# Kernel tuning notes

Measured on AMD Instinct MI355X. Metric: run time of the kernel, lower is better.

## Reference

```python
import jax, jax.numpy as jnp
import numpy as np

B, C, H, W = 4, 128, 64, 64
THITA = 1e-4


def conv1x1(x, w, b):
    # 1x1 conv + bias + ReLU; x:[B,Cin,H,W], w:[Cout,Cin], b:[Cout]
    return jax.nn.relu(jnp.einsum('bihw,oi->bohw', x, w) + b[None, :, None, None])


_CONV_SPECS = [
    ('neighbor', 2 * C, 4),
    ('pro_key', C, C), ('pro_val', C, C),
    ('lat_key', C, C), ('lat_val', C, C),
    ('tmp1', C, 2 * C),
    ('now1', C, 2),
    ('now_key', C, C), ('now_val', C, C),
    ('q', C, C), ('k', C, C), ('v', C, C),
]


def setup_inputs() -> dict:
    key = jax.random.key(0)
    ks = jax.random.split(key, 1 + 2 * len(_CONV_SPECS))
    inp = {'event': jax.random.normal(ks[0], (B, 6, H, W), dtype=jnp.float32)}
    i = 1
    for name, o, c in _CONV_SPECS:
        s = 1.0 / np.sqrt(c)
        inp['w_' + name] = jax.random.uniform(ks[i], (o, c), minval=-s, maxval=s, dtype=jnp.float32)
        inp['b_' + name] = jax.random.uniform(ks[i + 1], (o,), minval=-s, maxval=s, dtype=jnp.float32)
        i += 2
    return inp


def reference(event, w_neighbor, b_neighbor, w_pro_key, b_pro_key, w_pro_val, b_pro_val,
              w_lat_key, b_lat_key, w_lat_val, b_lat_val, w_tmp1, b_tmp1,
              w_now1, b_now1, w_now_key, b_now_key, w_now_val, b_now_val,
              w_q, b_q, w_k, b_k, w_v, b_v):
    pro, now, lat = event[:, 0:2], event[:, 2:4], event[:, 4:6]
    neigh = conv1x1(jnp.concatenate([pro, lat], axis=1), w_neighbor, b_neighbor)  # [B,2C,H,W]
    pro_key = conv1x1(neigh[:, :C], w_pro_key, b_pro_key)
    pro_val = conv1x1(neigh[:, C:], w_pro_val, b_pro_val)
    lat_key = conv1x1(neigh[:, :C], w_lat_key, b_lat_key)
    lat_val = conv1x1(neigh[:, C:], w_lat_val, b_lat_val)
    # NOTE: source applies conv_tmp1 (shared weights) to both key and val paths
    key_n = conv1x1(jnp.concatenate([pro_key, lat_key], axis=1), w_tmp1, b_tmp1)
    val_n = conv1x1(jnp.concatenate([pro_val, lat_val], axis=1), w_tmp1, b_tmp1)
    now_f = conv1x1(now, w_now1, b_now1)
    now_key = conv1x1(now_f, w_now_key, b_now_key)
    now_val = conv1x1(now_f, w_now_val, b_now_val)
    N = H * W
    q = conv1x1(key_n, w_q, b_q).reshape(B, C, N)          # proj_query pre-permute
    k = conv1x1(now_key, w_k, b_k).reshape(B, C, N)        # [B,C,N]
    attn = jax.nn.softmax(jnp.einsum('bcn,bcm->bnm', q, k), axis=-1)  # [B,N,N]
    v = conv1x1(val_n, w_v, b_v).reshape(B, C, N)
    out = jnp.einsum('bcm,bnm->bcn', v, attn).reshape(B, C, H, W)
    return THITA * out + now_val
```

## Files before the change

kernel.cpp:

```cpp
#include <hip/hip_runtime.h>

#define B_ 4
#define C_ 128
#define N_ 4096
#define LOG2E 1.44269504088896340736f

typedef __attribute__((ext_vector_type(8))) __bf16 bf16x8;
typedef __attribute__((ext_vector_type(16))) float f32x16;

#define SWZ(n) (((n) & 15) << 4)

__device__ __forceinline__ unsigned short cvb(float x) {
    return __builtin_bit_cast(unsigned short, (__bf16)x);
}
__device__ __forceinline__ unsigned pk2(float lo, float hi) {
    return (unsigned)cvb(lo) | ((unsigned)cvb(hi) << 16);
}
__device__ __forceinline__ float bfu(unsigned short u) {
    return __builtin_bit_cast(float, (unsigned)u << 16);
}
__device__ __forceinline__ float fexp2(float x) {
#if __has_builtin(__builtin_amdgcn_exp2f)
    return __builtin_amdgcn_exp2f(x);
#else
    float r;
    asm("v_exp_f32 %0, %1" : "=v"(r) : "v"(x));
    return r;
#endif
}
__device__ inline void gload_lds16(const void* g, void* l) {
    __builtin_amdgcn_global_load_lds(
        (const __attribute__((address_space(1))) unsigned int*)g,
        (__attribute__((address_space(3))) unsigned int*)l, 16, 0, 0);
}
__device__ __forceinline__ void plswapf(float& a, float& b) {
    asm volatile("v_permlane32_swap_b32 %0, %1" : "+v"(a), "+v"(b));
}
__device__ __forceinline__ void plswapu(unsigned& a, unsigned& b) {
    asm volatile("v_permlane32_swap_b32 %0, %1" : "+v"(a), "+v"(b));
}

__global__ __launch_bounds__(256) void k_wcvt(
        const float* pk, const float* lk, const float* pv, const float* lv,
        const float* t1, const float* nk, const float* nv,
        const float* q, const float* k, const float* v,
        const float* bpk, const float* blk, const float* bpv, const float* blv,
        const float* bnk, const float* bnv,
        unsigned short* Wk, unsigned short* Wv, unsigned short* Wt1,
        unsigned short* Wnow, unsigned short* Wq, unsigned short* Wkk,
        unsigned short* Wvv, float* bck, float* bcv, float* bcn) {
    int i = blockIdx.x * 256 + threadIdx.x;
    if (i < 22528) {
        int c = i;
        const float *s0, *s1 = nullptr;
        unsigned short* dst;
        int ks;
        if      (c < 4096)  { dst = Wk;   ks = 3; s0 = pk; s1 = lk; }
        else if (c < 8192)  { dst = Wv;   ks = 3; s0 = pv; s1 = lv; c -= 4096; }
        else if (c < 12288) { dst = Wt1;  ks = 4; s0 = t1;          c -= 8192; }
        else if (c < 16384) { dst = Wnow; ks = 3; s0 = nk; s1 = nv; c -= 12288; }
        else if (c < 18432) { dst = Wq;   ks = 3; s0 = q;           c -= 16384; }
        else if (c < 20480) { dst = Wkk;  ks = 3; s0 = k;           c -= 18432; }
        else                { dst = Wvv;  ks = 3; s0 = v;           c -= 20480; }
        int K = 16 << ks;
        int lane = c & 63, tile = c >> 6;
        int mt = tile >> ks, kt = tile & ((1 << ks) - 1);
        int row = mt * 32 + (lane & 31);
        int col = kt * 16 + (lane >> 5) * 8;
        const float* src = (s1 && row >= 128) ? (s1 + (size_t)(row - 128) * K + col)
                                              : (s0 + (size_t)row * K + col);
        unsigned short ov[8];
        #pragma unroll
        for (int j = 0; j < 8; ++j) ov[j] = cvb(src[j]);
        *(uint4*)(dst + (size_t)c * 8) = *(const uint4*)ov;
    }
    else if (i < 22784) { int j = i - 22528; bck[j] = j < 128 ? bpk[j] : blk[j - 128]; }
    else if (i < 23040) { int j = i - 22784; bcv[j] = j < 128 ? bpv[j] : blv[j - 128]; }
    else if (i < 23296) { int j = i - 23040; bcn[j] = j < 128 ? bnk[j] : bnv[j - 128]; }
}

template<int KSTEPS, int ROWB>
__device__ __forceinline__ f32x16 gtile(const char* Ab, int aChBase,
        const unsigned short* Wf, int mchunk, int nl, int h) {
    f32x16 acc;
    #pragma unroll
    for (int r = 0; r < 16; ++r) acc[r] = 0.f;
    const char* arow = Ab + nl * ROWB;
    const unsigned short* wb = Wf + ((size_t)mchunk * KSTEPS) * 512 + (nl + 32 * h) * 8;
    #pragma unroll
    for (int kk = 0; kk < KSTEPS; ++kk) {
        bf16x8 a = *(const bf16x8*)(arow + ((aChBase + kk * 32 + h * 16) ^ SWZ(nl)));
        bf16x8 wf = *(const bf16x8*)(wb + kk * 512);
        acc = __builtin_amdgcn_mfma_f32_32x32x16_bf16(a, wf, acc, 0, 0, 0);
    }
    return acc;
}

__device__ __forceinline__ void epi_lds(char* dst, int rowB, f32x16 acc,
        const float* bias, int m0, int nl, int h) {
    int m = m0 + nl;
    float bs = bias[m];
    #pragma unroll
    for (int r = 0; r < 16; ++r) {
        int n = (r & 3) + 8 * (r >> 2) + 4 * h;
        *(unsigned short*)(dst + n * rowB + ((m * 2) ^ SWZ(n))) =
            cvb(fmaxf(acc[r] + bs, 0.f));
    }
}

__device__ __forceinline__ void epi_nc(unsigned short* Y, f32x16 acc,
        const float* bias, float scale, int m0, int n0g, int b, int nl, int h) {
    int m = m0 + nl;
    float bs = bias[m];
    #pragma unroll
    for (int r = 0; r < 16; ++r) {
        int n = (r & 3) + 8 * (r >> 2) + 4 * h;
        Y[((size_t)b * N_ + n0g + n) * C_ + m] = cvb(fmaxf(acc[r] + bs, 0.f) * scale);
    }
}

__device__ __forceinline__ void epi_cn_b16(unsigned short* Y, f32x16 acc,
        const float* bias, int m0, int n0g, int b, int nl, int h) {
    int m = m0 + nl;
    float bs = bias[m];
    #pragma unroll
    for (int r2 = 0; r2 < 4; ++r2) {
        int nn = 8 * r2 + 4 * h;
        uint2 o;
        o.x = pk2(fmaxf(acc[4*r2+0] + bs, 0.f), fmaxf(acc[4*r2+1] + bs, 0.f));
        o.y = pk2(fmaxf(acc[4*r2+2] + bs, 0.f), fmaxf(acc[4*r2+3] + bs, 0.f));
        *(uint2*)(Y + ((size_t)b * C_ + m) * N_ + n0g + nn) = o;
    }
}

__device__ __forceinline__ void epi_cn_f32(float* Y, f32x16 acc,
        const float* bias, int m0, int n0g, int b, int nl, int h) {
    int m = m0 + nl;
    float bs = bias[m];
    #pragma unroll
    for (int r2 = 0; r2 < 4; ++r2) {
        int nn = 8 * r2 + 4 * h;
        float4 o;
        o.x = fmaxf(acc[4*r2+0] + bs, 0.f);
        o.y = fmaxf(acc[4*r2+1] + bs, 0.f);
        o.z = fmaxf(acc[4*r2+2] + bs, 0.f);
        o.w = fmaxf(acc[4*r2+3] + bs, 0.f);
        *(float4*)(Y + ((size_t)b * C_ + m) * N_ + n0g + nn) = o;
    }
}

__global__ __launch_bounds__(256) void k_chain(
        const float* __restrict__ ev, const float* __restrict__ w_nb,
        const float* __restrict__ b_nb, const float* __restrict__ w_n1,
        const float* __restrict__ b_n1,
        const unsigned short* __restrict__ Wk, const unsigned short* __restrict__ Wv,
        const unsigned short* __restrict__ Wt1, const unsigned short* __restrict__ Wnow,
        const unsigned short* __restrict__ Wq, const unsigned short* __restrict__ Wkk,
        const unsigned short* __restrict__ Wvv,
        const float* __restrict__ bck, const float* __restrict__ bcv,
        const float* __restrict__ bt1, const float* __restrict__ bcn,
        const float* __restrict__ bq, const float* __restrict__ bk,
        const float* __restrict__ bv,
        unsigned short* __restrict__ Qt, unsigned short* __restrict__ Kb,
        unsigned short* __restrict__ Vb, float* __restrict__ NowV) {
    __shared__ char lds[57344];
    char* NEIGH = lds;
    char* KCAT  = lds + 16384;
    char* VCAT  = lds + 32768;
    char* NOWF  = lds + 49152;
    char* KEYN  = lds;
    char* VALN  = lds + 8192;
    char* NOWK  = lds + 16384;

    const int t = threadIdx.x, lane = t & 63, w = t >> 6;
    const int nl = lane & 31, h = lane >> 5;
    const int b = blockIdx.y;
    const int n0g = blockIdx.x * 32;
    const int m0 = w * 32;
    const int mc = w;

    {
        int n = t & 31, grp = t >> 5;
        const float* evb = ev + (size_t)b * 6 * N_ + n0g + n;
        float e0 = evb[0], e1 = evb[N_], e4 = evb[4*N_], e5 = evb[5*N_];
        float e2 = evb[2*N_], e3 = evb[3*N_];
        int och0 = grp * 32;
        #pragma unroll
        for (int i = 0; i < 32; i += 4) {
            float r_[4];
            #pragma unroll
            for (int j = 0; j < 4; ++j) {
                int o = och0 + i + j;
                float4 w4 = *(const float4*)(w_nb + o * 4);
                r_[j] = fmaxf(b_nb[o] + w4.x*e0 + w4.y*e1 + w4.z*e4 + w4.w*e5, 0.f);
            }
            uint2 val; val.x = pk2(r_[0], r_[1]); val.y = pk2(r_[2], r_[3]);
            *(uint2*)(NEIGH + n * 512 + (((och0 + i) * 2) ^ SWZ(n))) = val;
        }
        int o0 = grp * 16;
        #pragma unroll
        for (int i = 0; i < 16; i += 4) {
            float r_[4];
            #pragma unroll
            for (int j = 0; j < 4; ++j) {
                int o = o0 + i + j;
                float2 w2 = *(const float2*)(w_n1 + o * 2);
                r_[j] = fmaxf(b_n1[o] + w2.x*e2 + w2.y*e3, 0.f);
            }
            uint2 val; val.x = pk2(r_[0], r_[1]); val.y = pk2(r_[2], r_[3]);
            *(uint2*)(NOWF + n * 256 + (((o0 + i) * 2) ^ SWZ(n))) = val;
        }
    }
    __syncthreads();

    {
        f32x16 a0 = gtile<8, 512>(NEIGH, 0,   Wk, mc,     nl, h);
        f32x16 a1 = gtile<8, 512>(NEIGH, 0,   Wk, mc + 4, nl, h);
        f32x16 a2 = gtile<8, 512>(NEIGH, 256, Wv, mc,     nl, h);
        f32x16 a3 = gtile<8, 512>(NEIGH, 256, Wv, mc + 4, nl, h);
        epi_lds(KCAT, 512, a0, bck, m0,       nl, h);
        epi_lds(KCAT, 512, a1, bck, m0 + 128, nl, h);
        epi_lds(VCAT, 512, a2, bcv, m0,       nl, h);
        epi_lds(VCAT, 512, a3, bcv, m0 + 128, nl, h);
    }
    __syncthreads();

    {
        f32x16 a0 = gtile<16, 512>(KCAT, 0, Wt1, mc, nl, h);
        f32x16 a1 = gtile<16, 512>(VCAT, 0, Wt1, mc, nl, h);
        epi_lds(KEYN, 256, a0, bt1, m0, nl, h);
        epi_lds(VALN, 256, a1, bt1, m0, nl, h);
    }
    __syncthreads();

    {
        f32x16 a0 = gtile<8, 256>(NOWF, 0, Wnow, mc,     nl, h);
        f32x16 a1 = gtile<8, 256>(NOWF, 0, Wnow, mc + 4, nl, h);
        epi_lds(NOWK, 256, a0, bcn, m0, nl, h);
        epi_cn_f32(NowV, a1, bcn + 128, m0, n0g, b, nl, h);
    }
    __syncthreads();

    {
        f32x16 aq = gtile<8, 256>(KEYN, 0, Wq,  mc, nl, h);
        f32x16 ak = gtile<8, 256>(NOWK, 0, Wkk, mc, nl, h);
        f32x16 av = gtile<8, 256>(VALN, 0, Wvv, mc, nl, h);
        epi_nc(Qt, aq, bq, LOG2E, m0, n0g, b, nl, h);
        epi_nc(Kb, ak, bk, 1.0f,  m0, n0g, b, nl, h);
        epi_cn_b16(Vb, av, bv, m0, n0g, b, nl, h);
    }
}

#define SPLIT 4
#define CHUNK 32

__global__ __launch_bounds__(128) void k_flashp(
        const unsigned short* __restrict__ Qt, const unsigned short* __restrict__ Kt,
        const unsigned short* __restrict__ Vb,
        unsigned short* __restrict__ Opb, float* __restrict__ ML) {
    __shared__ char stg[2][16384];
    const int t = threadIdx.x;
    const int lane = t & 63;
    const int nh = t >> 6;
    const int h = lane >> 5, nl = lane & 31;
    const int i_ = blockIdx.x;
    const int mpb = (i_ & 7) + 8 * ((i_ >> 3) & 1);
    const int ntile = i_ >> 4;
    const int mp = mpb >> 2, b = mpb & 3;
    const int n0 = ntile * 64 + nh * 32;
    const size_t bo = (size_t)b * N_ * C_;

    bf16x8 qf[8];
    {
        const char* qb = (const char*)(Qt + bo);
        #pragma unroll
        for (int kk = 0; kk < 8; ++kk)
            qf[kk] = *(const bf16x8*)(qb + (size_t)(n0 + nl) * 256 + kk*32 + h*16);
    }

    const char* ktb = (const char*)(Kt + bo);
    const char* vbb = (const char*)(Vb + bo);

    f32x16 oa[4];
    #pragma unroll
    for (int ss = 0; ss < 4; ++ss)
        #pragma unroll
        for (int r = 0; r < 16; ++r) oa[ss][r] = 0.f;
    float m_run = -1e30f, l_run = 0.f;

    const int swzK = (nl & 15) << 4;
    const int swzV = ((nl >> 1) & 7) << 4;

    auto stage = [&](int tile, int ph) {
        char* base = stg[ph];
        if (nh == 0) {
            const char* src = ktb + (size_t)tile * 8192;
            #pragma unroll
            for (int ii = 0; ii < 8; ++ii) {
                int L = ii*1024 + lane*16;
                int T = L ^ (((L >> 8) & 15) << 4);
                gload_lds16(src + T, base + ii*1024);
            }
        } else {
            const char* src = vbb + (size_t)tile * 64;
            #pragma unroll
            for (int ii = 0; ii < 8; ++ii) {
                int L = ii*1024 + lane*16;
                int T = L ^ (((L >> 7) & 7) << 4);
                int c = T >> 6, inner = T & 63;
                gload_lds16(src + (size_t)c * (N_*2) + inner, base + 8192 + ii*1024);
            }
        }
    };

    const int tb = mp * CHUNK;
    stage(tb, 0);
    stage(tb + 1, 1);

    for (int it = 0; it < CHUNK; ++it) {
        int ph = it & 1;
        if (it < CHUNK - 1) asm volatile("s_waitcnt vmcnt(8)" ::: "memory");
        else                asm volatile("s_waitcnt vmcnt(0)" ::: "memory");
        __builtin_amdgcn_s_barrier();
        __builtin_amdgcn_sched_barrier(0);
        const char* kb = stg[ph];
        const char* vb = kb + 8192;

        f32x16 s;
        #pragma unroll
        for (int r = 0; r < 16; ++r) s[r] = 0.f;
        __builtin_amdgcn_s_setprio(1);
        #pragma unroll
        for (int kk = 0; kk < 8; ++kk) {
            int y = nl*256 + kk*32 + h*16;
            bf16x8 a = *(const bf16x8*)(kb + (y ^ swzK));
            s = __builtin_amdgcn_mfma_f32_32x32x16_bf16(a, qf[kk], s, 0, 0, 0);
        }
        __builtin_amdgcn_s_setprio(0);

        float tm = fmaxf(fmaxf(fmaxf(s[0], s[1]), fmaxf(s[2], s[3])),
                         fmaxf(fmaxf(s[4], s[5]), fmaxf(s[6], s[7])));
        float tm2 = fmaxf(fmaxf(fmaxf(s[8], s[9]), fmaxf(s[10], s[11])),
                          fmaxf(fmaxf(s[12], s[13]), fmaxf(s[14], s[15])));
        tm = fmaxf(tm, tm2);
        { float x = tm, y = tm; plswapf(x, y); tm = fmaxf(x, y); }
        if (!__all(tm <= m_run + 8.f)) {
            float mn = fmaxf(m_run, tm);
            float sc = fexp2(m_run - mn);
            m_run = mn;
            l_run *= sc;
            #pragma unroll
            for (int ss = 0; ss < 4; ++ss)
                #pragma unroll
                for (int r = 0; r < 16; ++r) oa[ss][r] *= sc;
        }
        float p[16];
        float ls = 0.f;
        #pragma unroll
        for (int r = 0; r < 16; ++r) { p[r] = fexp2(s[r] - m_run); ls += p[r]; }
        { float x = ls, y = ls; plswapf(x, y); ls = x + y; }
        l_run += ls;

        unsigned pk_[8];
        #pragma unroll
        for (int q = 0; q < 8; ++q) pk_[q] = pk2(p[2*q], p[2*q+1]);
        unsigned a0 = pk_[0], a1 = pk_[1], b0 = pk_[2], b1 = pk_[3];
        plswapu(a0, b0); plswapu(a1, b1);
        unsigned c0 = pk_[4], c1 = pk_[5], d0 = pk_[6], d1 = pk_[7];
        plswapu(c0, d0); plswapu(c1, d1);
        typedef __attribute__((ext_vector_type(4))) unsigned u32x4;
        u32x4 uw0 = {a0, a1, b0, b1};
        u32x4 uw1 = {c0, c1, d0, d1};
        bf16x8 pf0 = __builtin_bit_cast(bf16x8, uw0);
        bf16x8 pf1 = __builtin_bit_cast(bf16x8, uw1);

        __builtin_amdgcn_s_setprio(1);
        #pragma unroll
        for (int ss = 0; ss < 4; ++ss) {
            int y0 = (32*ss + nl)*64 + h*16;
            bf16x8 va0 = *(const bf16x8*)(vb + (y0 ^ swzV));
            oa[ss] = __builtin_amdgcn_mfma_f32_32x32x16_bf16(va0, pf0, oa[ss], 0, 0, 0);
            bf16x8 va1 = *(const bf16x8*)(vb + ((y0 + 32) ^ swzV));
            oa[ss] = __builtin_amdgcn_mfma_f32_32x32x16_bf16(va1, pf1, oa[ss], 0, 0, 0);
        }
        __builtin_amdgcn_s_setprio(0);

        __builtin_amdgcn_sched_barrier(0);
        __builtin_amdgcn_s_barrier();
        if (it + 2 < CHUNK) stage(tb + it + 2, ph);
    }

    const size_t pb = (size_t)(mp * B_ + b) * 64 + ntile;
    if (h == 0) {
        ML[pb*128 +      nh*32 + nl] = m_run;
        ML[pb*128 + 64 + nh*32 + nl] = l_run;
    }
    unsigned short* dst = Opb + pb * 8192;
    #pragma unroll
    for (int ss = 0; ss < 4; ++ss)
        #pragma unroll
        for (int r = 0; r < 16; ++r) {
            int c = 32*ss + (r&3) + 8*(r>>2) + 4*h;
            dst[c*64 + nh*32 + nl] = cvb(oa[ss][r]);
        }
}

__global__ __launch_bounds__(256) void k_comb(const unsigned short* __restrict__ Opb,
        const float* __restrict__ ML, const float* __restrict__ NV,
        float* __restrict__ out) {
    const int t = threadIdx.x;
    const int ntile = blockIdx.x, b = blockIdx.y;
    const int n = t & 63, tq = t >> 6;
    float mj[SPLIT], lj[SPLIT], wj[SPLIT];
    #pragma unroll
    for (int j = 0; j < SPLIT; ++j) {
        size_t pb = (size_t)(j * B_ + b) * 64 + ntile;
        mj[j] = ML[pb*128 + n];
        lj[j] = ML[pb*128 + 64 + n];
    }
    float M = -1e30f;
    #pragma unroll
    for (int j = 0; j < SPLIT; ++j) M = fmaxf(M, mj[j]);
    float den = 0.f;
    #pragma unroll
    for (int j = 0; j < SPLIT; ++j) { wj[j] = fexp2(mj[j] - M); den += lj[j] * wj[j]; }
    float sc = 1e-4f / den;
    #pragma unroll 4
    for (int c = tq; c < C_; c += 4) {
        float v = 0.f;
        #pragma unroll
        for (int j = 0; j < SPLIT; ++j)
            v += bfu(Opb[((size_t)(j * B_ + b) * 64 + ntile) * 8192 + c*64 + n]) * wj[j];
        size_t gi = ((size_t)b * C_ + c) * N_ + ntile*64 + n;
        out[gi] = sc * v + NV[gi];
    }
}

extern "C" void kernel_launch(void* const* d_in, const int* in_sizes, int n_in,
                              void* d_out, int out_size, void* d_ws, size_t ws_size,
                              hipStream_t stream) {
    const float* ev   = (const float*)d_in[0];
    const float* w_nb = (const float*)d_in[1];  const float* b_nb = (const float*)d_in[2];
    const float* w_pk = (const float*)d_in[3];  const float* b_pk = (const float*)d_in[4];
    const float* w_pv = (const float*)d_in[5];  const float* b_pv = (const float*)d_in[6];
    const float* w_lk = (const float*)d_in[7];  const float* b_lk = (const float*)d_in[8];
    const float* w_lv = (const float*)d_in[9];  const float* b_lv = (const float*)d_in[10];
    const float* w_t1 = (const float*)d_in[11]; const float* b_t1 = (const float*)d_in[12];
    const float* w_n1 = (const float*)d_in[13]; const float* b_n1 = (const float*)d_in[14];
    const float* w_nk = (const float*)d_in[15]; const float* b_nk = (const float*)d_in[16];
    const float* w_nv = (const float*)d_in[17]; const float* b_nv = (const float*)d_in[18];
    const float* w_q  = (const float*)d_in[19]; const float* b_q  = (const float*)d_in[20];
    const float* w_k  = (const float*)d_in[21]; const float* b_k  = (const float*)d_in[22];
    const float* w_v  = (const float*)d_in[23]; const float* b_v  = (const float*)d_in[24];

    char* p = (char*)d_ws;
    unsigned short* Qt = (unsigned short*)p; p += (size_t)B_*N_*C_*2;
    unsigned short* Kb = (unsigned short*)p; p += (size_t)B_*N_*C_*2;
    unsigned short* Vb = (unsigned short*)p; p += (size_t)B_*C_*N_*2;
    float*          NowV = (float*)p;        p += (size_t)B_*C_*N_*4;
    unsigned short* Wk   = (unsigned short*)p; p += 32768*2;
    unsigned short* Wv   = (unsigned short*)p; p += 32768*2;
    unsigned short* Wt1  = (unsigned short*)p; p += 32768*2;
    unsigned short* Wnow = (unsigned short*)p; p += 32768*2;
    unsigned short* Wq   = (unsigned short*)p; p += 16384*2;
    unsigned short* Wkk  = (unsigned short*)p; p += 16384*2;
    unsigned short* Wvv  = (unsigned short*)p; p += 16384*2;
    float* bck = (float*)p; p += 256*4;
    float* bcv = (float*)p; p += 256*4;
    float* bcn = (float*)p; p += 256*4;
    p = (char*)(((size_t)p + 255) & ~(size_t)255);
    unsigned short* Opb = (unsigned short*)p; p += (size_t)SPLIT*B_*64*8192*2;
    float* ML = (float*)p; p += (size_t)SPLIT*B_*64*128*4;

    k_wcvt<<<dim3(91), dim3(256), 0, stream>>>(
        w_pk, w_lk, w_pv, w_lv, w_t1, w_nk, w_nv, w_q, w_k, w_v,
        b_pk, b_lk, b_pv, b_lv, b_nk, b_nv,
        Wk, Wv, Wt1, Wnow, Wq, Wkk, Wvv, bck, bcv, bcn);

    k_chain<<<dim3(N_/32, B_), dim3(256), 0, stream>>>(
        ev, w_nb, b_nb, w_n1, b_n1,
        Wk, Wv, Wt1, Wnow, Wq, Wkk, Wvv,
        bck, bcv, b_t1, bcn, b_q, b_k, b_v,
        Qt, Kb, Vb, NowV);

    k_flashp<<<dim3(N_/64 * SPLIT * B_), dim3(128), 0, stream>>>(Qt, Kb, Vb, Opb, ML);

    k_comb<<<dim3(N_/64, B_), dim3(256), 0, stream>>>(Opb, ML, NowV, (float*)d_out);
}
```

Measured before the change: 86.76 us.

## Double the KV split and restructure K/V staging with single-buffered V

```diff
diff --git a/kernel.cpp b/kernel.cpp
--- a/kernel.cpp
+++ b/kernel.cpp
@@ -251,22 +251,23 @@
     }
 }
 
-#define SPLIT 4
-#define CHUNK 32
+#define SPLIT 8
+#define CHUNK 16
 
 __global__ __launch_bounds__(128) void k_flashp(
         const unsigned short* __restrict__ Qt, const unsigned short* __restrict__ Kt,
         const unsigned short* __restrict__ Vb,
         unsigned short* __restrict__ Opb, float* __restrict__ ML) {
-    __shared__ char stg[2][16384];
+    __shared__ char stgK[2][8192];
+    __shared__ char stgV[8192];
     const int t = threadIdx.x;
     const int lane = t & 63;
     const int nh = t >> 6;
     const int h = lane >> 5, nl = lane & 31;
     const int i_ = blockIdx.x;
-    const int mpb = (i_ & 7) + 8 * ((i_ >> 3) & 1);
-    const int ntile = i_ >> 4;
-    const int mp = mpb >> 2, b = mpb & 3;
+    const int combo = i_ & 31;
+    const int ntile = i_ >> 5;
+    const int mp = combo >> 2, b = combo & 3;
     const int n0 = ntile * 64 + nh * 32;
     const size_t bo = (size_t)b * N_ * C_;
 
@@ -291,40 +292,41 @@
     const int swzK = (nl & 15) << 4;
     const int swzV = ((nl >> 1) & 7) << 4;
 
-    auto stage = [&](int tile, int ph) {
-        char* base = stg[ph];
-        if (nh == 0) {
-            const char* src = ktb + (size_t)tile * 8192;
-            #pragma unroll
-            for (int ii = 0; ii < 8; ++ii) {
-                int L = ii*1024 + lane*16;
-                int T = L ^ (((L >> 8) & 15) << 4);
-                gload_lds16(src + T, base + ii*1024);
-            }
-        } else {
-            const char* src = vbb + (size_t)tile * 64;
-            #pragma unroll
-            for (int ii = 0; ii < 8; ++ii) {
-                int L = ii*1024 + lane*16;
-                int T = L ^ (((L >> 7) & 7) << 4);
-                int c = T >> 6, inner = T & 63;
-                gload_lds16(src + (size_t)c * (N_*2) + inner, base + 8192 + ii*1024);
-            }
+    auto stageK = [&](int tile, int ph) {
+        const char* src = ktb + (size_t)tile * 8192;
+        char* base = stgK[ph];
+        #pragma unroll
+        for (int ii = 0; ii < 8; ++ii) {
+            int L = ii*1024 + lane*16;
+            int T = L ^ (((L >> 8) & 15) << 4);
+            gload_lds16(src + T, base + ii*1024);
         }
     };
+    auto stageV = [&](int tile) {
+        const char* src = vbb + (size_t)tile * 64;
+        #pragma unroll
+        for (int ii = 0; ii < 8; ++ii) {
+            int L = ii*1024 + lane*16;
+            int T = L ^ (((L >> 7) & 7) << 4);
+            int c = T >> 6, inner = T & 63;
+            gload_lds16(src + (size_t)c * (N_*2) + inner, stgV + ii*1024);
+        }
+    };
 
     const int tb = mp * CHUNK;
-    stage(tb, 0);
-    stage(tb + 1, 1);
+    if (nh == 0) stageK(tb, 0);
 
     for (int it = 0; it < CHUNK; ++it) {
         int ph = it & 1;
-        if (it < CHUNK - 1) asm volatile("s_waitcnt vmcnt(8)" ::: "memory");
-        else                asm volatile("s_waitcnt vmcnt(0)" ::: "memory");
+        if (nh == 1) stageV(tb + it);
+        else if (it + 1 < CHUNK) stageK(tb + it + 1, ph ^ 1);
+        if (nh == 0) {
+            if (it + 1 < CHUNK) asm volatile("s_waitcnt vmcnt(8)" ::: "memory");
+            else                asm volatile("s_waitcnt vmcnt(0)" ::: "memory");
+        }
         __builtin_amdgcn_s_barrier();
         __builtin_amdgcn_sched_barrier(0);
-        const char* kb = stg[ph];
-        const char* vb = kb + 8192;
+        const char* kb = stgK[ph];
 
         f32x16 s;
         #pragma unroll
@@ -374,20 +376,23 @@
         bf16x8 pf0 = __builtin_bit_cast(bf16x8, uw0);
         bf16x8 pf1 = __builtin_bit_cast(bf16x8, uw1);
 
+        if (nh == 1) asm volatile("s_waitcnt vmcnt(0)" ::: "memory");
+        __builtin_amdgcn_s_barrier();
+        __builtin_amdgcn_sched_barrier(0);
+
         __builtin_amdgcn_s_setprio(1);
         #pragma unroll
         for (int ss = 0; ss < 4; ++ss) {
             int y0 = (32*ss + nl)*64 + h*16;
-            bf16x8 va0 = *(const bf16x8*)(vb + (y0 ^ swzV));
+            bf16x8 va0 = *(const bf16x8*)(stgV + (y0 ^ swzV));
             oa[ss] = __builtin_amdgcn_mfma_f32_32x32x16_bf16(va0, pf0, oa[ss], 0, 0, 0);
-            bf16x8 va1 = *(const bf16x8*)(vb + ((y0 + 32) ^ swzV));
+            bf16x8 va1 = *(const bf16x8*)(stgV + ((y0 + 32) ^ swzV));
             oa[ss] = __builtin_amdgcn_mfma_f32_32x32x16_bf16(va1, pf1, oa[ss], 0, 0, 0);
         }
         __builtin_amdgcn_s_setprio(0);
 
         __builtin_amdgcn_sched_barrier(0);
         __builtin_amdgcn_s_barrier();
-        if (it + 2 < CHUNK) stage(tb + it + 2, ph);
     }
 
     const size_t pb = (size_t)(mp * B_ + b) * 64 + ntile;
```

After: 130.3 us. +50.2%, slower.
